# Performance work log

Hardware: AMD Instinct MI355X
Metric: run time of the kernel (lower is better)

Reference implementation:

```python
import jax, jax.numpy as jnp
import numpy as np

N_NODES = 50000
N_EDGES = 800000
D_IN = 128
H = 4
F = 16


def setup_inputs() -> dict:
    key = jax.random.key(0)
    k1, k2, k3, k4 = jax.random.split(key, 4)
    feat = jax.random.normal(k1, (N_NODES, D_IN), dtype=jnp.float32)
    W = jax.random.normal(k2, (D_IN, H * F), dtype=jnp.float32) / np.sqrt(D_IN)
    src = jax.random.randint(k3, (N_EDGES,), 0, N_NODES, dtype=jnp.int32)
    dst = jax.random.randint(k4, (N_EDGES,), 0, N_NODES, dtype=jnp.int32)
    return {"feat": feat, "W": W, "src": src, "dst": dst}


def reference(feat, W, src, dst):
    # Project: [N, D_in] @ [D_in, H*F] -> [N, H, F]
    ft = (feat @ W).reshape(N_NODES, H, F)
    # Per-edge dot-product scores, scaled: [E, H]
    e = jnp.einsum('ehf,ehf->eh', ft[src], ft[dst]) / np.sqrt(F).astype(np.float32)
    # Segment (per-destination) softmax over incoming edges
    seg_max = jax.ops.segment_max(e, dst, num_segments=N_NODES)  # [N, H]
    ex = jnp.exp(e - seg_max[dst])
    denom = jax.ops.segment_sum(ex, dst, num_segments=N_NODES)  # [N, H]
    sa = ex / denom[dst]  # [E, H]
    # Weighted scatter-sum of source features: [N, H, F]
    msgs = ft[src] * sa[:, :, None]
    out = jax.ops.segment_sum(msgs, dst, num_segments=N_NODES)
    return out
```

## Files before the change

kernel.cpp:

```cpp
#include <hip/hip_runtime.h>
#include <hip/hip_fp16.h>

#define N_NODES 50000
#define N_EDGES 800000
#define D_IN 128
#define HH 4
#define FF 16
#define HF 64
#define NBUCKETS 196
#define BCAP 4608
#define CHUNK 2048
#define NBIN_BLOCKS ((N_EDGES + CHUNK - 1) / CHUNK)
#define GEMM_BLOCKS ((N_NODES + 63) / 64)
#define SORT_K ((BCAP + 255) / 256)

struct __align__(8) Half4 { __half2 a, b; };

typedef _Float16 half2_v __attribute__((ext_vector_type(2)));
struct __align__(8) H4 { half2_v a, b; };

__device__ __forceinline__ float dot4h(H4 a, H4 v) {
#if __has_builtin(__builtin_amdgcn_fdot2)
    return __builtin_amdgcn_fdot2(a.a, v.a,
           __builtin_amdgcn_fdot2(a.b, v.b, 0.0f, false), false);
#else
    return (float)a.a[0] * (float)v.a[0] + (float)a.a[1] * (float)v.a[1]
         + (float)a.b[0] * (float)v.b[0] + (float)a.b[1] * (float)v.b[1];
#endif
}

__device__ __forceinline__ int block_excl_scan(int val, int* wsum) {
    int lane = threadIdx.x & 63;
    int wave = threadIdx.x >> 6;
    int incl = val;
#pragma unroll
    for (int off = 1; off < 64; off <<= 1) {
        int t = __shfl_up(incl, off, 64);
        if (lane >= off) incl += t;
    }
    if (lane == 63) wsum[wave] = incl;
    __syncthreads();
    if (threadIdx.x == 0) {
        int a = 0;
#pragma unroll
        for (int w = 0; w < 4; ++w) { int t = wsum[w]; wsum[w] = a; a += t; }
    }
    __syncthreads();
    return incl + wsum[wave] - val;
}

union SmemU {
    struct {
        float As[64][132];
        float Bs[D_IN][HF];
    } g;
    struct {
        int hist[256], offs[256], cur[256], gbase[256];
        int wsum[4];
        int lrec[CHUNK];
    } b;
};

__global__ __launch_bounds__(256, 2) void gemm_bin_kernel(const float* __restrict__ feat,
                                                          const float* __restrict__ W,
                                                          const int* __restrict__ src,
                                                          const int* __restrict__ dst,
                                                          __half* __restrict__ fth,
                                                          int* __restrict__ gcur,
                                                          int* __restrict__ recs) {
    __shared__ SmemU smem;
    int tid = threadIdx.x;

    if (blockIdx.x < NBIN_BLOCKS) {
        int e0 = blockIdx.x * CHUNK;
        int n = N_EDGES - e0; if (n > CHUNK) n = CHUNK;

        smem.b.hist[tid] = 0;
        __syncthreads();

        int myrec[CHUNK / 256];
        int myb[CHUNK / 256];
#pragma unroll
        for (int k = 0; k < CHUNK / 256; ++k) {
            int idx = tid + k * 256;
            myb[k] = -1;
            if (idx < n) {
                int s = src[e0 + idx];
                int d = dst[e0 + idx];
                int b = d >> 8;
                myrec[k] = s | ((d & 255) << 16) | (b << 24);
                myb[k] = b;
                atomicAdd(&smem.b.hist[b], 1);
            }
        }
        __syncthreads();

        int val = smem.b.hist[tid];
        int excl = block_excl_scan(val, smem.b.wsum);
        smem.b.offs[tid] = excl;
        smem.b.cur[tid] = excl;
        if (val > 0) smem.b.gbase[tid] = atomicAdd(&gcur[tid], val);
        __syncthreads();

#pragma unroll
        for (int k = 0; k < CHUNK / 256; ++k) {
            if (myb[k] >= 0) {
                int p = atomicAdd(&smem.b.cur[myb[k]], 1);
                smem.b.lrec[p] = myrec[k];
            }
        }
        __syncthreads();

        for (int i = tid; i < n; i += 256) {
            int r = smem.b.lrec[i];
            int b = (r >> 24) & 255;
            int pos = smem.b.gbase[b] + (i - smem.b.offs[b]);
            if (pos < BCAP) recs[(size_t)b * BCAP + pos] = r;
        }
    } else {
        int gb = blockIdx.x - NBIN_BLOCKS;
        {
            const float4* W4 = (const float4*)W;
            float4* B4 = (float4*)smem.g.Bs;
#pragma unroll
            for (int i = 0; i < 8; ++i) {
                int idx = tid + 256 * i;
                B4[idx] = W4[idx];
            }
        }
        {
            int row0 = gb * 64;
            const float4* F4 = (const float4*)feat;
#pragma unroll
            for (int i = 0; i < 8; ++i) {
                int idx = tid + 256 * i;
                int r = idx >> 5;
                int c4 = idx & 31;
                float4 v = make_float4(0.f, 0.f, 0.f, 0.f);
                int row = row0 + r;
                if (row < N_NODES) v = F4[(size_t)row * 32 + c4];
                *(float4*)&smem.g.As[r][c4 * 4] = v;
            }
        }
        __syncthreads();

        const int tr = tid >> 4;
        const int tc = tid & 15;

        float acc[4][4] = {};
#pragma unroll 8
        for (int k = 0; k < D_IN; k += 4) {
            float av[4][4], bv[4][4];
#pragma unroll
            for (int i = 0; i < 4; ++i) {
                float4 a = *(const float4*)&smem.g.As[tr * 4 + i][k];
                av[i][0] = a.x; av[i][1] = a.y; av[i][2] = a.z; av[i][3] = a.w;
            }
#pragma unroll
            for (int j = 0; j < 4; ++j) {
                float4 b = *(const float4*)&smem.g.Bs[k + j][tc * 4];
                bv[j][0] = b.x; bv[j][1] = b.y; bv[j][2] = b.z; bv[j][3] = b.w;
            }
#pragma unroll
            for (int i = 0; i < 4; ++i)
#pragma unroll
                for (int j = 0; j < 4; ++j)
#pragma unroll
                    for (int c = 0; c < 4; ++c)
                        acc[i][c] = fmaf(av[i][j], bv[j][c], acc[i][c]);
        }

        int row0 = gb * 64;
#pragma unroll
        for (int i = 0; i < 4; ++i) {
            int row = row0 + tr * 4 + i;
            if (row < N_NODES) {
                Half4 h;
                h.a = __floats2half2_rn(acc[i][0], acc[i][1]);
                h.b = __floats2half2_rn(acc[i][2], acc[i][3]);
                *(Half4*)&fth[(size_t)row * HF + tc * 4] = h;
            }
        }
    }
}

__global__ __launch_bounds__(256) void sort_kernel(const int* __restrict__ gcur,
                                                   const int* __restrict__ recs,
                                                   unsigned short* __restrict__ csr,
                                                   int2* __restrict__ rows) {
    __shared__ int lhist[256];
    __shared__ int lcur[256];
    __shared__ int wsum[4];

    int tid = threadIdx.x;
    int b = blockIdx.x;
    int cnt = gcur[b]; if (cnt > BCAP) cnt = BCAP;
    const int* rp = recs + (size_t)b * BCAP;

    lhist[tid] = 0;
    __syncthreads();

    int rk[SORT_K];
#pragma unroll
    for (int k = 0; k < SORT_K; ++k) {
        int i = tid + k * 256;
        bool valid = i < cnt;
        rk[k] = valid ? rp[i] : 0;
        if (valid) atomicAdd(&lhist[(rk[k] >> 16) & 255], 1);
    }
    __syncthreads();

    int val = lhist[tid];
    int excl = block_excl_scan(val, wsum);
    lcur[tid] = excl;
    __syncthreads();

    int base = b * BCAP;
#pragma unroll
    for (int k = 0; k < SORT_K; ++k) {
        int i = tid + k * 256;
        if (i < cnt) {
            int p = atomicAdd(&lcur[(rk[k] >> 16) & 255], 1);
            csr[base + p] = (unsigned short)(rk[k] & 0xFFFF);
        }
    }

    int node = (b << 8) + tid;
    if (node < N_NODES) rows[node] = make_int2(base + excl, base + excl + val);
}

__global__ __launch_bounds__(256) void gather_kernel(const __half* __restrict__ fth,
                                                     const int2* __restrict__ rows,
                                                     const unsigned short* __restrict__ csr,
                                                     float* __restrict__ out) {
    int node = __builtin_amdgcn_readfirstlane(blockIdx.x * 4 + (threadIdx.x >> 6));
    int lane = threadIdx.x & 63;
    int g = lane >> 4;
    int hl = lane & 15;

    int2 be = rows[node];
    int beg = be.x;
    int end = be.y;

    H4 a = *(const H4*)&fth[(size_t)node * HF + 4 * hl];

    float acc0 = 0.f, acc1 = 0.f, acc2 = 0.f, acc3 = 0.f, lsum = 0.f;

    for (int i = beg; i < end; i += 8) {
        int idx0 = i + g;
        int idx1 = i + 4 + g;
        bool act0 = idx0 < end;
        bool act1 = idx1 < end;
        int s0 = csr[act0 ? idx0 : beg];
        int s1 = csr[act1 ? idx1 : beg];
        H4 v0 = *(const H4*)&fth[(size_t)s0 * HF + 4 * hl];
        H4 v1 = *(const H4*)&fth[(size_t)s1 * HF + 4 * hl];

        float p0 = dot4h(a, v0);
        float p1 = dot4h(a, v1);
        p0 += __shfl_xor(p0, 1, 64);  p1 += __shfl_xor(p1, 1, 64);
        p0 += __shfl_xor(p0, 2, 64);  p1 += __shfl_xor(p1, 2, 64);

        float w0 = act0 ? __expf(p0 * 0.25f) : 0.0f;
        float w1 = act1 ? __expf(p1 * 0.25f) : 0.0f;

        acc0 = fmaf(w0, (float)v0.a[0], acc0);
        acc1 = fmaf(w0, (float)v0.a[1], acc1);
        acc2 = fmaf(w0, (float)v0.b[0], acc2);
        acc3 = fmaf(w0, (float)v0.b[1], acc3);
        acc0 = fmaf(w1, (float)v1.a[0], acc0);
        acc1 = fmaf(w1, (float)v1.a[1], acc1);
        acc2 = fmaf(w1, (float)v1.b[0], acc2);
        acc3 = fmaf(w1, (float)v1.b[1], acc3);
        lsum += w0 + w1;
    }

    acc0 += __shfl_xor(acc0, 16, 64);  acc0 += __shfl_xor(acc0, 32, 64);
    acc1 += __shfl_xor(acc1, 16, 64);  acc1 += __shfl_xor(acc1, 32, 64);
    acc2 += __shfl_xor(acc2, 16, 64);  acc2 += __shfl_xor(acc2, 32, 64);
    acc3 += __shfl_xor(acc3, 16, 64);  acc3 += __shfl_xor(acc3, 32, 64);
    lsum += __shfl_xor(lsum, 16, 64);  lsum += __shfl_xor(lsum, 32, 64);

    if (lane < 16) {
        float inv = (lsum > 0.0f) ? 1.0f / lsum : 0.0f;
        *(float4*)&out[(size_t)node * HF + 4 * hl] =
            make_float4(acc0 * inv, acc1 * inv, acc2 * inv, acc3 * inv);
    }
}

extern "C" void kernel_launch(void* const* d_in, const int* in_sizes, int n_in,
                              void* d_out, int out_size, void* d_ws, size_t ws_size,
                              hipStream_t stream) {
    const float* feat = (const float*)d_in[0];
    const float* W = (const float*)d_in[1];
    const int* src = (const int*)d_in[2];
    const int* dst = (const int*)d_in[3];
    float* out = (float*)d_out;

    __half* fth = (__half*)d_ws;
    int* recs = (int*)(fth + (size_t)N_NODES * HF);
    unsigned short* csr = (unsigned short*)(recs + (size_t)NBUCKETS * BCAP);
    int2* rows = (int2*)(csr + (size_t)NBUCKETS * BCAP);
    int* gcur = (int*)(rows + N_NODES);

    hipMemsetAsync(gcur, 0, NBUCKETS * sizeof(int), stream);
    gemm_bin_kernel<<<NBIN_BLOCKS + GEMM_BLOCKS, 256, 0, stream>>>(feat, W, src, dst,
                                                                   fth, gcur, recs);
    sort_kernel<<<NBUCKETS, 256, 0, stream>>>(gcur, recs, csr, rows);
    gather_kernel<<<N_NODES * 64 / 256, 256, 0, stream>>>(fth, rows, csr, out);
}
```

Measured before the change: 142.5 us.

## Scatter bin records directly and unroll gather loop to four edges

```diff
diff --git a/kernel.cpp b/kernel.cpp
--- a/kernel.cpp
+++ b/kernel.cpp
@@ -55,9 +55,7 @@
         float Bs[D_IN][HF];
     } g;
     struct {
-        int hist[256], offs[256], cur[256], gbase[256];
-        int wsum[4];
-        int lrec[CHUNK];
+        int hist[256], cur[256], gbase[256];
     } b;
 };
 
@@ -96,26 +94,17 @@
         __syncthreads();
 
         int val = smem.b.hist[tid];
-        int excl = block_excl_scan(val, smem.b.wsum);
-        smem.b.offs[tid] = excl;
-        smem.b.cur[tid] = excl;
+        smem.b.cur[tid] = 0;
         if (val > 0) smem.b.gbase[tid] = atomicAdd(&gcur[tid], val);
         __syncthreads();
 
 #pragma unroll
         for (int k = 0; k < CHUNK / 256; ++k) {
-            if (myb[k] >= 0) {
-                int p = atomicAdd(&smem.b.cur[myb[k]], 1);
-                smem.b.lrec[p] = myrec[k];
-            }
-        }
-        __syncthreads();
-
-        for (int i = tid; i < n; i += 256) {
-            int r = smem.b.lrec[i];
-            int b = (r >> 24) & 255;
-            int pos = smem.b.gbase[b] + (i - smem.b.offs[b]);
-            if (pos < BCAP) recs[(size_t)b * BCAP + pos] = r;
+            int b = myb[k];
+            if (b >= 0) {
+                int pos = smem.b.gbase[b] + atomicAdd(&smem.b.cur[b], 1);
+                if (pos < BCAP) recs[(size_t)b * BCAP + pos] = myrec[k];
+            }
         }
     } else {
         int gb = blockIdx.x - NBIN_BLOCKS;
@@ -246,33 +235,34 @@
 
     float acc0 = 0.f, acc1 = 0.f, acc2 = 0.f, acc3 = 0.f, lsum = 0.f;
 
-    for (int i = beg; i < end; i += 8) {
-        int idx0 = i + g;
-        int idx1 = i + 4 + g;
-        bool act0 = idx0 < end;
-        bool act1 = idx1 < end;
-        int s0 = csr[act0 ? idx0 : beg];
-        int s1 = csr[act1 ? idx1 : beg];
-        H4 v0 = *(const H4*)&fth[(size_t)s0 * HF + 4 * hl];
-        H4 v1 = *(const H4*)&fth[(size_t)s1 * HF + 4 * hl];
-
-        float p0 = dot4h(a, v0);
-        float p1 = dot4h(a, v1);
-        p0 += __shfl_xor(p0, 1, 64);  p1 += __shfl_xor(p1, 1, 64);
-        p0 += __shfl_xor(p0, 2, 64);  p1 += __shfl_xor(p1, 2, 64);
-
-        float w0 = act0 ? __expf(p0 * 0.25f) : 0.0f;
-        float w1 = act1 ? __expf(p1 * 0.25f) : 0.0f;
-
-        acc0 = fmaf(w0, (float)v0.a[0], acc0);
-        acc1 = fmaf(w0, (float)v0.a[1], acc1);
-        acc2 = fmaf(w0, (float)v0.b[0], acc2);
-        acc3 = fmaf(w0, (float)v0.b[1], acc3);
-        acc0 = fmaf(w1, (float)v1.a[0], acc0);
-        acc1 = fmaf(w1, (float)v1.a[1], acc1);
-        acc2 = fmaf(w1, (float)v1.b[0], acc2);
-        acc3 = fmaf(w1, (float)v1.b[1], acc3);
-        lsum += w0 + w1;
+    for (int i = beg; i < end; i += 16) {
+        int s[4];
+        bool act[4];
+        H4 v[4];
+        float p[4];
+#pragma unroll
+        for (int u = 0; u < 4; ++u) {
+            int idx = i + 4 * u + g;
+            act[u] = idx < end;
+            s[u] = csr[act[u] ? idx : beg];
+        }
+#pragma unroll
+        for (int u = 0; u < 4; ++u) v[u] = *(const H4*)&fth[(size_t)s[u] * HF + 4 * hl];
+#pragma unroll
+        for (int u = 0; u < 4; ++u) p[u] = dot4h(a, v[u]);
+#pragma unroll
+        for (int u = 0; u < 4; ++u) p[u] += __shfl_xor(p[u], 1, 64);
+#pragma unroll
+        for (int u = 0; u < 4; ++u) p[u] += __shfl_xor(p[u], 2, 64);
+#pragma unroll
+        for (int u = 0; u < 4; ++u) {
+            float w = act[u] ? __expf(p[u] * 0.25f) : 0.0f;
+            acc0 = fmaf(w, (float)v[u].a[0], acc0);
+            acc1 = fmaf(w, (float)v[u].a[1], acc1);
+            acc2 = fmaf(w, (float)v[u].b[0], acc2);
+            acc3 = fmaf(w, (float)v[u].b[1], acc3);
+            lsum += w;
+        }
     }
 
     acc0 += __shfl_xor(acc0, 16, 64);  acc0 += __shfl_xor(acc0, 32, 64);
```

New measurement: 140.3 us. No clear change (-1.6%).
